# Kernel tuning notes

Measured on AMD Instinct MI355X. Metric: run time of the kernel, lower is better.

Reference implementation:

```python
import jax, jax.numpy as jnp
import numpy as np
import math

B, S_IN, S_OUT, D_IN, D_OUT, G = 8, 1024, 1024, 96, 96, 8
LN_EPS = 1e-5


def setup_inputs() -> dict:
    key = jax.random.key(0)
    k_x, k_m, k_p, k_l = jax.random.split(key, 4)
    x = jax.random.normal(k_x, (B, S_IN, D_IN), dtype=jnp.float32)
    M = jax.random.uniform(k_m, (D_OUT, D_IN), minval=-0.5, maxval=0.5, dtype=jnp.float32)
    P = jax.random.uniform(k_p, (D_OUT, D_OUT, G), minval=-0.1, maxval=0.1, dtype=jnp.float32)
    Linker = jax.random.uniform(k_l, (S_IN, S_OUT), minval=-0.1, maxval=0.1, dtype=jnp.float32)
    gamma = jnp.ones((D_OUT,), dtype=jnp.float32)
    beta = jnp.zeros((D_OUT,), dtype=jnp.float32)
    return {"x": x, "M": M, "P": P, "Linker": Linker, "gamma": gamma, "beta": beta}


def _layer_norm(z, gamma, beta):
    mu = jnp.mean(z, axis=-1, keepdims=True)
    var = jnp.mean(jnp.square(z - mu), axis=-1, keepdims=True)
    return (z - mu) * jax.lax.rsqrt(var + LN_EPS) * gamma + beta


def reference(x, M, P, Linker, gamma, beta):
    # Z = x @ M^T, then LayerNorm over feature dim
    Z0 = jnp.einsum('bsj,ij->bsi', x, M)           # (B, S_in, D_out)
    Z = _layer_norm(Z0, gamma, beta)
    # periods[i,j,g] = i*(D_out*G) + j*G + g + 2
    periods = (jnp.arange(D_OUT * D_OUT * G, dtype=jnp.float32)
               .reshape(D_OUT, D_OUT, G) + 2.0)
    k = jnp.arange(S_IN, dtype=jnp.float32)
    # phi[s,i,j,g] = cos(2*pi*s / periods[i,j,g])
    phi = jnp.cos((2.0 * math.pi) * k[:, None, None, None] / periods[None])
    # fuse basis reduction: W[s,i,j] = sum_g P[i,j,g] * phi[s,i,j,g]
    W = jnp.einsum('sijg,ijg->sij', phi, P)        # (S_in, D_out, D_out)
    # T[b,s,i] = sum_j Z[b,s,j] * W[s,i,j]
    T = jnp.einsum('bsj,sij->bsi', Z, W)           # (B, S_in, D_out)
    # sequence transform via Linker
    U = jnp.einsum('bsi,st->bti', T, Linker)       # (B, S_out, D_out)
    # shared residual: x @ M^T (pre-LN) through the same Linker
    residual = jnp.einsum('bsi,st->bti', Z0, Linker)
    return U + residual
```

## Files before the change

### kernel.cpp

```cpp
#include <hip/hip_runtime.h>
#include <cstdint>
#include <cstddef>

#define BSTRIDE 98304

typedef __attribute__((ext_vector_type(8))) short short8;
typedef __attribute__((ext_vector_type(4))) float f32x4;

__device__ __forceinline__ uint16_t f2bf(float x) {
    uint32_t u = __float_as_uint(x);
    return (uint16_t)((u + 0x7FFF + ((u >> 16) & 1)) >> 16);
}
__device__ __forceinline__ float bf2f(uint16_t b) {
    return __uint_as_float(((uint32_t)b) << 16);
}
__device__ __forceinline__ float cosrev(float x) {
    return __builtin_amdgcn_cosf(x);
}

union SmemA {
    struct {
        union {
            float M[96][97];
            struct { float zb[16][97]; float ps1[16][8];
                     float ps2[16][8]; float stats[16][2]; } ln;
        } m;
        float xs[16][96];
    } a;
    struct { float T[64][65]; } kl;
};

__global__ __launch_bounds__(384, 4) void kA(
    const float* __restrict__ x, const float* __restrict__ M,
    const float* __restrict__ L,
    const float* __restrict__ gamma, const float* __restrict__ beta,
    float* __restrict__ Z0, float* __restrict__ Z, uint16_t* __restrict__ Lt)
{
    __shared__ SmemA sm;
    const int t  = threadIdx.x;
    const int bx = blockIdx.x;

    if (bx >= 512) {
        const int bx2 = bx - 512;
        const int s0 = (bx2 & 15) * 64, t0 = (bx2 >> 4) * 64;
        if (t < 64) {
            for (int r = 0; r < 64; ++r)
                sm.kl.T[r][t] = L[(size_t)(s0 + r) * 1024 + t0 + t];
        }
        __syncthreads();
        if (t < 64) {
            uint16_t* orow = Lt + (size_t)(t0 + t) * 1024 + s0;
            #pragma unroll
            for (int c4 = 0; c4 < 16; ++c4) {
                uint32_t u01 = (uint32_t)f2bf(sm.kl.T[c4*4+0][t]) |
                               ((uint32_t)f2bf(sm.kl.T[c4*4+1][t]) << 16);
                uint32_t u23 = (uint32_t)f2bf(sm.kl.T[c4*4+2][t]) |
                               ((uint32_t)f2bf(sm.kl.T[c4*4+3][t]) << 16);
                uint2 o; o.x = u01; o.y = u23;
                *(uint2*)(orow + c4 * 4) = o;
            }
        }
        return;
    }

    const int R0 = bx * 16;
    const int b  = R0 >> 10;
    const int sb = R0 & 1023;

    #pragma unroll
    for (int k = 0; k < 6; ++k) {
        int mm = t + 384 * k;
        int i = mm / 24, j0 = (mm % 24) * 4;
        float4 v = *(const float4*)(M + (size_t)i * 96 + j0);
        sm.a.m.M[i][j0]   = v.x; sm.a.m.M[i][j0+1] = v.y;
        sm.a.m.M[i][j0+2] = v.z; sm.a.m.M[i][j0+3] = v.w;
    }
    {
        int row = t / 24, j0 = (t % 24) * 4;
        float4 v = *(const float4*)(x + (size_t)(R0 + row) * 96 + j0);
        *(float4*)&sm.a.xs[row][j0] = v;
    }
    __syncthreads();

    const int e = t % 96;
    const int q = t / 96;
    float acc[4] = {0.f, 0.f, 0.f, 0.f};
    for (int j0 = 0; j0 < 96; j0 += 4) {
        float m0 = sm.a.m.M[e][j0+0], m1 = sm.a.m.M[e][j0+1];
        float m2 = sm.a.m.M[e][j0+2], m3 = sm.a.m.M[e][j0+3];
        #pragma unroll
        for (int rr = 0; rr < 4; ++rr) {
            float4 xv = *(const float4*)&sm.a.xs[q * 4 + rr][j0];
            acc[rr] = fmaf(m0, xv.x, fmaf(m1, xv.y,
                      fmaf(m2, xv.z, fmaf(m3, xv.w, acc[rr]))));
        }
    }
    __syncthreads();
    #pragma unroll
    for (int rr = 0; rr < 4; ++rr) sm.a.m.ln.zb[q * 4 + rr][e] = acc[rr];
    __syncthreads();

    if (t < 128) {
        int r = t >> 3, seg = t & 7;
        float s1 = 0.f, s2 = 0.f;
        #pragma unroll
        for (int k = 0; k < 12; ++k) {
            float v = sm.a.m.ln.zb[r][seg * 12 + k];
            s1 += v; s2 += v * v;
        }
        sm.a.m.ln.ps1[r][seg] = s1; sm.a.m.ln.ps2[r][seg] = s2;
    }
    __syncthreads();
    if (t < 16) {
        float s1 = 0.f, s2 = 0.f;
        #pragma unroll
        for (int k = 0; k < 8; ++k) { s1 += sm.a.m.ln.ps1[t][k]; s2 += sm.a.m.ln.ps2[t][k]; }
        float mu  = s1 * (1.f / 96.f);
        float var = s2 * (1.f / 96.f) - mu * mu;
        sm.a.m.ln.stats[t][0] = mu;
        sm.a.m.ln.stats[t][1] = rsqrtf(var + 1e-5f);
    }
    __syncthreads();

    {
        float gm = gamma[e], bt = beta[e];
        #pragma unroll
        for (int rr = 0; rr < 4; ++rr) {
            int r = q * 4 + rr;
            float z  = acc[rr];
            float mu = sm.a.m.ln.stats[r][0], rs = sm.a.m.ln.stats[r][1];
            size_t o = (size_t)(sb + r) * 768 + (size_t)b * 96 + e;
            Z0[o] = z;
            Z[o]  = (z - mu) * rs * gm + bt;
        }
    }
}

struct SmemB {
    float    zs[8][8][100];
    uint16_t W[8][12][104];
    uint16_t stage[12][8][8];
};

__global__ __launch_bounds__(384, 4) void kB(
    const float* __restrict__ P, const float* __restrict__ Z,
    const float* __restrict__ Z0, uint16_t* __restrict__ Vt)
{
    __shared__ SmemB sm;
    const int t  = threadIdx.x;
    const int sg = blockIdx.x >> 3;
    const int ih = blockIdx.x & 7;
    const int s0 = sg * 8;
    const int i0 = ih * 12;

    #pragma unroll
    for (int k = 0; k < 4; ++k) {
        int c = t + 384 * k;
        int elem = c * 4;
        int sp = elem / 768, rem = elem - sp * 768;
        int bb = rem / 96,  j0 = rem - bb * 96;
        float4 v = *(const float4*)(Z + (size_t)s0 * 768 + elem);
        *(float4*)&sm.zs[sp][bb][j0] = v;
    }

    {
        const int j   = t % 96;
        const int iqb = t / 96;
        const float sf = (float)s0;
        #pragma unroll 1
        for (int kk = 0; kk < 3; ++kk) {
            const int ip = kk * 4 + iqb;
            const int ig = i0 + ip;
            const float* Pp = P + ((size_t)ig * 96 + j) * 8;
            float4 pa = *(const float4*)(Pp);
            float4 pb = *(const float4*)(Pp + 4);
            float pv[8] = {pa.x, pa.y, pa.z, pa.w, pb.x, pb.y, pb.z, pb.w};
            float base = (float)((ig * 96 + j) * 8 + 2);
            float c[8], cp[8], tc[8];
            #pragma unroll
            for (int g = 0; g < 8; ++g) {
                float inv = __builtin_amdgcn_rcpf(base + (float)g);
                tc[g] = 2.0f * cosrev(inv);
                c[g]  = cosrev(__builtin_amdgcn_fractf(sf * inv));
                cp[g] = cosrev(__builtin_amdgcn_fractf((sf - 1.0f) * inv));
            }
            #pragma unroll
            for (int sp = 0; sp < 8; ++sp) {
                float w = 0.f;
                #pragma unroll
                for (int g = 0; g < 8; ++g) w = fmaf(pv[g], c[g], w);
                sm.W[sp][ip][j] = f2bf(w);
                #pragma unroll
                for (int g = 0; g < 8; ++g) {
                    float cn = fmaf(tc[g], c[g], -cp[g]);
                    cp[g] = c[g]; c[g] = cn;
                }
            }
        }
    }
    __syncthreads();

    {
        const int s2  = t / 48;
        const int rem = t % 48;
        const int ipq = rem / 8;
        const int bb  = rem % 8;
        const int ia  = ipq * 2, ib = ia + 1;
        float accA = 0.f, accB = 0.f;
        const uint16_t* w0 = &sm.W[s2][ia][0];
        const uint16_t* w1 = &sm.W[s2][ib][0];
        const float*    zz = &sm.zs[s2][bb][0];
        #pragma unroll 3
        for (int j0 = 0; j0 < 96; j0 += 8) {
            short8 wa = *(const short8*)(w0 + j0);
            short8 wb = *(const short8*)(w1 + j0);
            float4 z0 = *(const float4*)(zz + j0);
            float4 z1 = *(const float4*)(zz + j0 + 4);
            accA = fmaf(bf2f((uint16_t)wa[0]), z0.x, accA);
            accB = fmaf(bf2f((uint16_t)wb[0]), z0.x, accB);
            accA = fmaf(bf2f((uint16_t)wa[1]), z0.y, accA);
            accB = fmaf(bf2f((uint16_t)wb[1]), z0.y, accB);
            accA = fmaf(bf2f((uint16_t)wa[2]), z0.z, accA);
            accB = fmaf(bf2f((uint16_t)wb[2]), z0.z, accB);
            accA = fmaf(bf2f((uint16_t)wa[3]), z0.w, accA);
            accB = fmaf(bf2f((uint16_t)wb[3]), z0.w, accB);
            accA = fmaf(bf2f((uint16_t)wa[4]), z1.x, accA);
            accB = fmaf(bf2f((uint16_t)wb[4]), z1.x, accB);
            accA = fmaf(bf2f((uint16_t)wa[5]), z1.y, accA);
            accB = fmaf(bf2f((uint16_t)wb[5]), z1.y, accB);
            accA = fmaf(bf2f((uint16_t)wa[6]), z1.z, accA);
            accB = fmaf(bf2f((uint16_t)wb[6]), z1.z, accB);
            accA = fmaf(bf2f((uint16_t)wa[7]), z1.w, accA);
            accB = fmaf(bf2f((uint16_t)wb[7]), z1.w, accB);
        }
        float2 r2 = *(const float2*)(Z0 + (size_t)(s0 + s2) * 768 + bb * 96 + i0 + ia);
        sm.stage[ia][bb][s2] = f2bf(accA + r2.x);
        sm.stage[ib][bb][s2] = f2bf(accB + r2.y);
    }
    __syncthreads();

    if (t < 96) {
        int ip = t >> 3, bb = t & 7;
        uint4 v = *(const uint4*)&sm.stage[ip][bb][0];
        *(uint4*)(Vt + ((size_t)bb * 96 + i0 + ip) * 1024 + s0) = v;
    }
}

__global__ __launch_bounds__(256, 4) void k3_mfma(
    const uint16_t* __restrict__ Lt, const uint16_t* __restrict__ Vt,
    float* __restrict__ out)
{
    __shared__ float racc[3][64][13];
    const int lane = threadIdx.x & 63;
    const int kw   = threadIdx.x >> 6;
    const int m    = lane & 15;
    const int quad = lane >> 4;
    const int t0   = blockIdx.x * 16;
    const int b    = blockIdx.y;
    const int ih   = blockIdx.z;

    const uint16_t* Lp = Lt + (size_t)(t0 + m) * 1024 + kw * 256 + quad * 8;
    const uint16_t* Vp = Vt + ((size_t)b * 96 + ih * 48 + m) * 1024 + kw * 256 + quad * 8;

    f32x4 acc[3];
    #pragma unroll
    for (int ii = 0; ii < 3; ++ii) acc[ii] = (f32x4){0.f, 0.f, 0.f, 0.f};

    short8 a = *(const short8*)Lp;
    short8 bv[3];
    #pragma unroll
    for (int ii = 0; ii < 3; ++ii)
        bv[ii] = *(const short8*)(Vp + (size_t)ii * 16 * 1024);

    for (int kc = 0; kc < 7; ++kc) {
        short8 an = *(const short8*)(Lp + (kc + 1) * 32);
        short8 bn[3];
        #pragma unroll
        for (int ii = 0; ii < 3; ++ii)
            bn[ii] = *(const short8*)(Vp + (size_t)ii * 16 * 1024 + (kc + 1) * 32);
        #pragma unroll
        for (int ii = 0; ii < 3; ++ii)
            acc[ii] = __builtin_amdgcn_mfma_f32_16x16x32_bf16(a, bv[ii], acc[ii], 0, 0, 0);
        a = an;
        #pragma unroll
        for (int ii = 0; ii < 3; ++ii) bv[ii] = bn[ii];
    }
    #pragma unroll
    for (int ii = 0; ii < 3; ++ii)
        acc[ii] = __builtin_amdgcn_mfma_f32_16x16x32_bf16(a, bv[ii], acc[ii], 0, 0, 0);

    if (kw > 0) {
        #pragma unroll
        for (int ii = 0; ii < 3; ++ii)
            #pragma unroll
            for (int r = 0; r < 4; ++r)
                racc[kw - 1][lane][ii * 4 + r] = acc[ii][r];
    }
    __syncthreads();
    if (kw == 0) {
        float* po = out + (size_t)b * BSTRIDE;
        #pragma unroll
        for (int ii = 0; ii < 3; ++ii)
            #pragma unroll
            for (int r = 0; r < 4; ++r)
                po[(size_t)(t0 + quad * 4 + r) * 96 + ih * 48 + ii * 16 + m] =
                    acc[ii][r] + racc[0][lane][ii * 4 + r] +
                    racc[1][lane][ii * 4 + r] + racc[2][lane][ii * 4 + r];
    }
}

extern "C" void kernel_launch(void* const* d_in, const int* in_sizes, int n_in,
                              void* d_out, int out_size, void* d_ws, size_t ws_size,
                              hipStream_t stream)
{
    const float* x     = (const float*)d_in[0];
    const float* M     = (const float*)d_in[1];
    const float* P     = (const float*)d_in[2];
    const float* Lnk   = (const float*)d_in[3];
    const float* gamma = (const float*)d_in[4];
    const float* beta  = (const float*)d_in[5];
    float* out = (float*)d_out;

    uint8_t* ws = (uint8_t*)d_ws;
    uint16_t* Lt = (uint16_t*)ws;
    uint16_t* Vt = (uint16_t*)(ws + 2097152);
    float*    Z0 = (float*)(ws + 3670016);
    float*    Z  = (float*)(ws + 6815744);

    kA<<<768, 384, 0, stream>>>(x, M, Lnk, gamma, beta, Z0, Z, Lt);
    kB<<<1024, 384, 0, stream>>>(P, Z, Z0, Vt);
    k3_mfma<<<dim3(64, 8, 2), 256, 0, stream>>>(Lt, Vt, out);
}
```

Baseline: 112.1 us.

## Fuse projection/LayerNorm kernel with W-basis contraction kernel via shared memory

Merges the x@M^T + LayerNorm kernel and the W-construction/contraction kernel into one kernel. Each block now handles 4 sequence positions across all 8 batches and half of the output features, so Z and Z0 stay in shared memory instead of going through global memory. This drops one launch and the Z/Z0 round trip. In exchange, M is reloaded and the projection recomputed per block pair, and the occupancy hint drops from 4 to 3 blocks per SM.

New measurement: 125.4 us. +11.9%, slower.

```diff
diff --git a/kernel.cpp b/kernel.cpp
--- a/kernel.cpp
+++ b/kernel.cpp
@@ -14,29 +14,27 @@
 __device__ __forceinline__ float bf2f(uint16_t b) {
     return __uint_as_float(((uint32_t)b) << 16);
 }
-__device__ __forceinline__ float cosrev(float x) {
-    return __builtin_amdgcn_cosf(x);
-}
-
-union SmemA {
+
+union SmemU {
     struct {
-        union {
-            float M[96][97];
-            struct { float zb[16][97]; float ps1[16][8];
-                     float ps2[16][8]; float stats[16][2]; } ln;
-        } m;
-        float xs[16][96];
-    } a;
+        union { float M[96][97]; uint16_t W[4][48][104]; } mw;
+        union { float xs[4][8][96]; uint16_t stage[48][8][4]; } xst;
+        float zr[4][8][97];
+        float zs[4][8][100];
+        float ps1[32][8];
+        float ps2[32][8];
+        float stats[32][2];
+    } c;
     struct { float T[64][65]; } kl;
 };
 
-__global__ __launch_bounds__(384, 4) void kA(
+__global__ __launch_bounds__(384, 3) void kAB(
     const float* __restrict__ x, const float* __restrict__ M,
-    const float* __restrict__ L,
+    const float* __restrict__ P, const float* __restrict__ L,
     const float* __restrict__ gamma, const float* __restrict__ beta,
-    float* __restrict__ Z0, float* __restrict__ Z, uint16_t* __restrict__ Lt)
+    uint16_t* __restrict__ Lt, uint16_t* __restrict__ Vt)
 {
-    __shared__ SmemA sm;
+    __shared__ SmemU sm;
     const int t  = threadIdx.x;
     const int bx = blockIdx.x;
 
@@ -63,133 +61,104 @@
         return;
     }
 
-    const int R0 = bx * 16;
-    const int b  = R0 >> 10;
-    const int sb = R0 & 1023;
+    const int gg = bx >> 1;
+    const int h  = bx & 1;
+    const int s0 = gg * 4;
+    const int i0 = h * 48;
 
     #pragma unroll
     for (int k = 0; k < 6; ++k) {
         int mm = t + 384 * k;
         int i = mm / 24, j0 = (mm % 24) * 4;
         float4 v = *(const float4*)(M + (size_t)i * 96 + j0);
-        sm.a.m.M[i][j0]   = v.x; sm.a.m.M[i][j0+1] = v.y;
-        sm.a.m.M[i][j0+2] = v.z; sm.a.m.M[i][j0+3] = v.w;
-    }
-    {
-        int row = t / 24, j0 = (t % 24) * 4;
-        float4 v = *(const float4*)(x + (size_t)(R0 + row) * 96 + j0);
-        *(float4*)&sm.a.xs[row][j0] = v;
+        sm.c.mw.M[i][j0]   = v.x; sm.c.mw.M[i][j0+1] = v.y;
+        sm.c.mw.M[i][j0+2] = v.z; sm.c.mw.M[i][j0+3] = v.w;
+    }
+    {
+        float4* xf = (float4*)&sm.c.xst.xs[0][0][0];
+        #pragma unroll
+        for (int r = 0; r < 2; ++r) {
+            int c = t + 384 * r;
+            int elem = c * 4;
+            int sp = elem / 768, rem = elem - sp * 768;
+            int bb = rem / 96,  j0 = rem - bb * 96;
+            xf[c] = *(const float4*)(x + (size_t)bb * BSTRIDE +
+                                     (size_t)(s0 + sp) * 96 + j0);
+        }
     }
     __syncthreads();
 
     const int e = t % 96;
     const int q = t / 96;
-    float acc[4] = {0.f, 0.f, 0.f, 0.f};
+    float acc[8] = {0.f,0.f,0.f,0.f,0.f,0.f,0.f,0.f};
     for (int j0 = 0; j0 < 96; j0 += 4) {
-        float m0 = sm.a.m.M[e][j0+0], m1 = sm.a.m.M[e][j0+1];
-        float m2 = sm.a.m.M[e][j0+2], m3 = sm.a.m.M[e][j0+3];
-        #pragma unroll
-        for (int rr = 0; rr < 4; ++rr) {
-            float4 xv = *(const float4*)&sm.a.xs[q * 4 + rr][j0];
-            acc[rr] = fmaf(m0, xv.x, fmaf(m1, xv.y,
-                      fmaf(m2, xv.z, fmaf(m3, xv.w, acc[rr]))));
-        }
-    }
-    __syncthreads();
-    #pragma unroll
-    for (int rr = 0; rr < 4; ++rr) sm.a.m.ln.zb[q * 4 + rr][e] = acc[rr];
-    __syncthreads();
-
-    if (t < 128) {
+        float m0 = sm.c.mw.M[e][j0+0], m1 = sm.c.mw.M[e][j0+1];
+        float m2 = sm.c.mw.M[e][j0+2], m3 = sm.c.mw.M[e][j0+3];
+        #pragma unroll
+        for (int bb = 0; bb < 8; ++bb) {
+            float4 xv = *(const float4*)&sm.c.xst.xs[q][bb][j0];
+            acc[bb] = fmaf(m0, xv.x, fmaf(m1, xv.y,
+                      fmaf(m2, xv.z, fmaf(m3, xv.w, acc[bb]))));
+        }
+    }
+    #pragma unroll
+    for (int bb = 0; bb < 8; ++bb) sm.c.zr[q][bb][e] = acc[bb];
+    __syncthreads();
+
+    if (t < 256) {
         int r = t >> 3, seg = t & 7;
+        const float* zp = &sm.c.zr[0][0][0] + r * 97 + seg * 12;
         float s1 = 0.f, s2 = 0.f;
         #pragma unroll
-        for (int k = 0; k < 12; ++k) {
-            float v = sm.a.m.ln.zb[r][seg * 12 + k];
-            s1 += v; s2 += v * v;
-        }
-        sm.a.m.ln.ps1[r][seg] = s1; sm.a.m.ln.ps2[r][seg] = s2;
-    }
-    __syncthreads();
-    if (t < 16) {
+        for (int k = 0; k < 12; ++k) { float v = zp[k]; s1 += v; s2 += v * v; }
+        sm.c.ps1[r][seg] = s1; sm.c.ps2[r][seg] = s2;
+    }
+    __syncthreads();
+    if (t < 32) {
         float s1 = 0.f, s2 = 0.f;
         #pragma unroll
-        for (int k = 0; k < 8; ++k) { s1 += sm.a.m.ln.ps1[t][k]; s2 += sm.a.m.ln.ps2[t][k]; }
+        for (int k = 0; k < 8; ++k) { s1 += sm.c.ps1[t][k]; s2 += sm.c.ps2[t][k]; }
         float mu  = s1 * (1.f / 96.f);
         float var = s2 * (1.f / 96.f) - mu * mu;
-        sm.a.m.ln.stats[t][0] = mu;
-        sm.a.m.ln.stats[t][1] = rsqrtf(var + 1e-5f);
+        sm.c.stats[t][0] = mu;
+        sm.c.stats[t][1] = rsqrtf(var + 1e-5f);
     }
     __syncthreads();
 
     {
         float gm = gamma[e], bt = beta[e];
         #pragma unroll
-        for (int rr = 0; rr < 4; ++rr) {
-            int r = q * 4 + rr;
-            float z  = acc[rr];
-            float mu = sm.a.m.ln.stats[r][0], rs = sm.a.m.ln.stats[r][1];
-            size_t o = (size_t)(sb + r) * 768 + (size_t)b * 96 + e;
-            Z0[o] = z;
-            Z[o]  = (z - mu) * rs * gm + bt;
-        }
-    }
-}
-
-struct SmemB {
-    float    zs[8][8][100];
-    uint16_t W[8][12][104];
-    uint16_t stage[12][8][8];
-};
-
-__global__ __launch_bounds__(384, 4) void kB(
-    const float* __restrict__ P, const float* __restrict__ Z,
-    const float* __restrict__ Z0, uint16_t* __restrict__ Vt)
-{
-    __shared__ SmemB sm;
-    const int t  = threadIdx.x;
-    const int sg = blockIdx.x >> 3;
-    const int ih = blockIdx.x & 7;
-    const int s0 = sg * 8;
-    const int i0 = ih * 12;
-
-    #pragma unroll
-    for (int k = 0; k < 4; ++k) {
-        int c = t + 384 * k;
-        int elem = c * 4;
-        int sp = elem / 768, rem = elem - sp * 768;
-        int bb = rem / 96,  j0 = rem - bb * 96;
-        float4 v = *(const float4*)(Z + (size_t)s0 * 768 + elem);
-        *(float4*)&sm.zs[sp][bb][j0] = v;
-    }
-
-    {
-        const int j   = t % 96;
-        const int iqb = t / 96;
-        const float sf = (float)s0;
-        #pragma unroll 1
-        for (int kk = 0; kk < 3; ++kk) {
-            const int ip = kk * 4 + iqb;
+        for (int bb = 0; bb < 8; ++bb) {
+            float mu = sm.c.stats[q * 8 + bb][0], rs = sm.c.stats[q * 8 + bb][1];
+            sm.c.zs[q][bb][e] = (acc[bb] - mu) * rs * gm + bt;
+        }
+    }
+    {
+        const float sf  = (float)s0;
+        const float sm1 = sf - 1.0f;
+        #pragma unroll 2
+        for (int kk = 0; kk < 12; ++kk) {
+            const int ip = kk * 4 + q;
             const int ig = i0 + ip;
-            const float* Pp = P + ((size_t)ig * 96 + j) * 8;
+            const float* Pp = P + ((size_t)ig * 96 + e) * 8;
             float4 pa = *(const float4*)(Pp);
             float4 pb = *(const float4*)(Pp + 4);
             float pv[8] = {pa.x, pa.y, pa.z, pa.w, pb.x, pb.y, pb.z, pb.w};
-            float base = (float)((ig * 96 + j) * 8 + 2);
+            float base = (float)((ig * 96 + e) * 8 + 2);
             float c[8], cp[8], tc[8];
             #pragma unroll
             for (int g = 0; g < 8; ++g) {
                 float inv = __builtin_amdgcn_rcpf(base + (float)g);
-                tc[g] = 2.0f * cosrev(inv);
-                c[g]  = cosrev(__builtin_amdgcn_fractf(sf * inv));
-                cp[g] = cosrev(__builtin_amdgcn_fractf((sf - 1.0f) * inv));
+                tc[g] = 2.0f * __builtin_amdgcn_cosf(inv);
+                c[g]  = __builtin_amdgcn_cosf(__builtin_amdgcn_fractf(sf  * inv));
+                cp[g] = __builtin_amdgcn_cosf(__builtin_amdgcn_fractf(sm1 * inv));
             }
             #pragma unroll
-            for (int sp = 0; sp < 8; ++sp) {
+            for (int sp = 0; sp < 4; ++sp) {
                 float w = 0.f;
                 #pragma unroll
                 for (int g = 0; g < 8; ++g) w = fmaf(pv[g], c[g], w);
-                sm.W[sp][ip][j] = f2bf(w);
+                sm.c.mw.W[sp][ip][e] = f2bf(w);
                 #pragma unroll
                 for (int g = 0; g < 8; ++g) {
                     float cn = fmaf(tc[g], c[g], -cp[g]);
@@ -201,48 +170,67 @@
     __syncthreads();
 
     {
-        const int s2  = t / 48;
-        const int rem = t % 48;
-        const int ipq = rem / 8;
-        const int bb  = rem % 8;
-        const int ia  = ipq * 2, ib = ia + 1;
-        float accA = 0.f, accB = 0.f;
-        const uint16_t* w0 = &sm.W[s2][ia][0];
-        const uint16_t* w1 = &sm.W[s2][ib][0];
-        const float*    zz = &sm.zs[s2][bb][0];
+        const int s2  = t / 96;
+        const int rem = t % 96;
+        const int ipq = rem >> 3;
+        const int bb  = rem & 7;
+        const int ia  = ipq * 4;
+        float a0 = 0.f, a1 = 0.f, a2 = 0.f, a3 = 0.f;
+        const uint16_t* w0 = &sm.c.mw.W[s2][ia][0];
+        const float*    zz = &sm.c.zs[s2][bb][0];
         #pragma unroll 3
         for (int j0 = 0; j0 < 96; j0 += 8) {
             short8 wa = *(const short8*)(w0 + j0);
-            short8 wb = *(const short8*)(w1 + j0);
+            short8 wb = *(const short8*)(w0 + 104 + j0);
+            short8 wc = *(const short8*)(w0 + 208 + j0);
+            short8 wd = *(const short8*)(w0 + 312 + j0);
             float4 z0 = *(const float4*)(zz + j0);
             float4 z1 = *(const float4*)(zz + j0 + 4);
-            accA = fmaf(bf2f((uint16_t)wa[0]), z0.x, accA);
-            accB = fmaf(bf2f((uint16_t)wb[0]), z0.x, accB);
-            accA = fmaf(bf2f((uint16_t)wa[1]), z0.y, accA);
-            accB = fmaf(bf2f((uint16_t)wb[1]), z0.y, accB);
-            accA = fmaf(bf2f((uint16_t)wa[2]), z0.z, accA);
-            accB = fmaf(bf2f((uint16_t)wb[2]), z0.z, accB);
-            accA = fmaf(bf2f((uint16_t)wa[3]), z0.w, accA);
-            accB = fmaf(bf2f((uint16_t)wb[3]), z0.w, accB);
-            accA = fmaf(bf2f((uint16_t)wa[4]), z1.x, accA);
-            accB = fmaf(bf2f((uint16_t)wb[4]), z1.x, accB);
-            accA = fmaf(bf2f((uint16_t)wa[5]), z1.y, accA);
-            accB = fmaf(bf2f((uint16_t)wb[5]), z1.y, accB);
-            accA = fmaf(bf2f((uint16_t)wa[6]), z1.z, accA);
-            accB = fmaf(bf2f((uint16_t)wb[6]), z1.z, accB);
-            accA = fmaf(bf2f((uint16_t)wa[7]), z1.w, accA);
-            accB = fmaf(bf2f((uint16_t)wb[7]), z1.w, accB);
-        }
-        float2 r2 = *(const float2*)(Z0 + (size_t)(s0 + s2) * 768 + bb * 96 + i0 + ia);
-        sm.stage[ia][bb][s2] = f2bf(accA + r2.x);
-        sm.stage[ib][bb][s2] = f2bf(accB + r2.y);
-    }
-    __syncthreads();
-
-    if (t < 96) {
+            a0 = fmaf(bf2f((uint16_t)wa[0]), z0.x, a0);
+            a1 = fmaf(bf2f((uint16_t)wb[0]), z0.x, a1);
+            a2 = fmaf(bf2f((uint16_t)wc[0]), z0.x, a2);
+            a3 = fmaf(bf2f((uint16_t)wd[0]), z0.x, a3);
+            a0 = fmaf(bf2f((uint16_t)wa[1]), z0.y, a0);
+            a1 = fmaf(bf2f((uint16_t)wb[1]), z0.y, a1);
+            a2 = fmaf(bf2f((uint16_t)wc[1]), z0.y, a2);
+            a3 = fmaf(bf2f((uint16_t)wd[1]), z0.y, a3);
+            a0 = fmaf(bf2f((uint16_t)wa[2]), z0.z, a0);
+            a1 = fmaf(bf2f((uint16_t)wb[2]), z0.z, a1);
+            a2 = fmaf(bf2f((uint16_t)wc[2]), z0.z, a2);
+            a3 = fmaf(bf2f((uint16_t)wd[2]), z0.z, a3);
+            a0 = fmaf(bf2f((uint16_t)wa[3]), z0.w, a0);
+            a1 = fmaf(bf2f((uint16_t)wb[3]), z0.w, a1);
+            a2 = fmaf(bf2f((uint16_t)wc[3]), z0.w, a2);
+            a3 = fmaf(bf2f((uint16_t)wd[3]), z0.w, a3);
+            a0 = fmaf(bf2f((uint16_t)wa[4]), z1.x, a0);
+            a1 = fmaf(bf2f((uint16_t)wb[4]), z1.x, a1);
+            a2 = fmaf(bf2f((uint16_t)wc[4]), z1.x, a2);
+            a3 = fmaf(bf2f((uint16_t)wd[4]), z1.x, a3);
+            a0 = fmaf(bf2f((uint16_t)wa[5]), z1.y, a0);
+            a1 = fmaf(bf2f((uint16_t)wb[5]), z1.y, a1);
+            a2 = fmaf(bf2f((uint16_t)wc[5]), z1.y, a2);
+            a3 = fmaf(bf2f((uint16_t)wd[5]), z1.y, a3);
+            a0 = fmaf(bf2f((uint16_t)wa[6]), z1.z, a0);
+            a1 = fmaf(bf2f((uint16_t)wb[6]), z1.z, a1);
+            a2 = fmaf(bf2f((uint16_t)wc[6]), z1.z, a2);
+            a3 = fmaf(bf2f((uint16_t)wd[6]), z1.z, a3);
+            a0 = fmaf(bf2f((uint16_t)wa[7]), z1.w, a0);
+            a1 = fmaf(bf2f((uint16_t)wb[7]), z1.w, a1);
+            a2 = fmaf(bf2f((uint16_t)wc[7]), z1.w, a2);
+            a3 = fmaf(bf2f((uint16_t)wd[7]), z1.w, a3);
+        }
+        const float* zrow = &sm.c.zr[s2][bb][i0 + ia];
+        sm.c.xst.stage[ia+0][bb][s2] = f2bf(a0 + zrow[0]);
+        sm.c.xst.stage[ia+1][bb][s2] = f2bf(a1 + zrow[1]);
+        sm.c.xst.stage[ia+2][bb][s2] = f2bf(a2 + zrow[2]);
+        sm.c.xst.stage[ia+3][bb][s2] = f2bf(a3 + zrow[3]);
+    }
+    __syncthreads();
+
+    {
         int ip = t >> 3, bb = t & 7;
-        uint4 v = *(const uint4*)&sm.stage[ip][bb][0];
-        *(uint4*)(Vt + ((size_t)bb * 96 + i0 + ip) * 1024 + s0) = v;
+        uint2 v = *(const uint2*)&sm.c.xst.stage[ip][bb][0];
+        *(uint2*)(Vt + ((size_t)bb * 96 + i0 + ip) * 1024 + s0) = v;
     }
 }
 
@@ -324,10 +312,7 @@
     uint8_t* ws = (uint8_t*)d_ws;
     uint16_t* Lt = (uint16_t*)ws;
     uint16_t* Vt = (uint16_t*)(ws + 2097152);
-    float*    Z0 = (float*)(ws + 3670016);
-    float*    Z  = (float*)(ws + 6815744);
-
-    kA<<<768, 384, 0, stream>>>(x, M, Lnk, gamma, beta, Z0, Z, Lt);
-    kB<<<1024, 384, 0, stream>>>(P, Z, Z0, Vt);
+
+    kAB    <<<768, 384, 0, stream>>>(x, M, P, Lnk, gamma, beta, Lt, Vt);
     k3_mfma<<<dim3(64, 8, 2), 256, 0, stream>>>(Lt, Vt, out);
 }
```

## Halve kB sequence tile, prefetch P/Z into registers, one output per thread

Applied to the files above, without the earlier changes.

kB now processes 4 sequence positions per block instead of 8, doubling the grid to 2048 blocks and raising the launch-bounds occupancy hint to 6. P coefficients and Z tiles are loaded into registers before the cosine recurrence so global latency overlaps the trig work. The residual load is issued before the barrier. The contraction now computes one output per thread with four independent accumulators, which breaks the FMA dependency chain. The trade-off is that the per-block cosine setup (rcp and cos per g) is amortized over fewer positions, so total trig work roughly doubles.

Result: slower. 135.9 us (+21.2%).

```diff
diff --git a/kernel.cpp b/kernel.cpp
--- a/kernel.cpp
+++ b/kernel.cpp
@@ -13,9 +13,6 @@
 }
 __device__ __forceinline__ float bf2f(uint16_t b) {
     return __uint_as_float(((uint32_t)b) << 16);
-}
-__device__ __forceinline__ float cosrev(float x) {
-    return __builtin_amdgcn_cosf(x);
 }
 
 union SmemA {
@@ -137,55 +134,60 @@
 }
 
 struct SmemB {
-    float    zs[8][8][100];
-    uint16_t W[8][12][104];
-    uint16_t stage[12][8][8];
+    float    zs[4][8][100];
+    uint16_t W[4][12][100];
+    uint16_t stage[12][8][4];
 };
 
-__global__ __launch_bounds__(384, 4) void kB(
+__global__ __launch_bounds__(384, 6) void kB(
     const float* __restrict__ P, const float* __restrict__ Z,
     const float* __restrict__ Z0, uint16_t* __restrict__ Vt)
 {
     __shared__ SmemB sm;
     const int t  = threadIdx.x;
-    const int sg = blockIdx.x >> 3;
-    const int ih = blockIdx.x & 7;
-    const int s0 = sg * 8;
+    const int sg = blockIdx.x & 255;
+    const int ih = blockIdx.x >> 8;
+    const int s0 = sg * 4;
     const int i0 = ih * 12;
 
-    #pragma unroll
-    for (int k = 0; k < 4; ++k) {
-        int c = t + 384 * k;
-        int elem = c * 4;
-        int sp = elem / 768, rem = elem - sp * 768;
-        int bb = rem / 96,  j0 = rem - bb * 96;
-        float4 v = *(const float4*)(Z + (size_t)s0 * 768 + elem);
-        *(float4*)&sm.zs[sp][bb][j0] = v;
+    const int j   = t % 96;
+    const int iqb = t / 96;
+
+    float4 pA[3], pB[3];
+    #pragma unroll
+    for (int kk = 0; kk < 3; ++kk) {
+        const int ig = i0 + kk * 4 + iqb;
+        const float* Pp = P + ((size_t)ig * 96 + j) * 8;
+        pA[kk] = *(const float4*)(Pp);
+        pB[kk] = *(const float4*)(Pp + 4);
+    }
+    float4 zreg[2];
+    #pragma unroll
+    for (int r = 0; r < 2; ++r) {
+        int c = t + 384 * r;
+        zreg[r] = *(const float4*)(Z + (size_t)s0 * 768 + (size_t)c * 4);
     }
 
     {
-        const int j   = t % 96;
-        const int iqb = t / 96;
-        const float sf = (float)s0;
+        const float sf  = (float)s0;
+        const float sm1 = sf - 1.0f;
         #pragma unroll 1
         for (int kk = 0; kk < 3; ++kk) {
             const int ip = kk * 4 + iqb;
             const int ig = i0 + ip;
-            const float* Pp = P + ((size_t)ig * 96 + j) * 8;
-            float4 pa = *(const float4*)(Pp);
-            float4 pb = *(const float4*)(Pp + 4);
-            float pv[8] = {pa.x, pa.y, pa.z, pa.w, pb.x, pb.y, pb.z, pb.w};
+            float pv[8] = {pA[kk].x, pA[kk].y, pA[kk].z, pA[kk].w,
+                           pB[kk].x, pB[kk].y, pB[kk].z, pB[kk].w};
             float base = (float)((ig * 96 + j) * 8 + 2);
             float c[8], cp[8], tc[8];
             #pragma unroll
             for (int g = 0; g < 8; ++g) {
                 float inv = __builtin_amdgcn_rcpf(base + (float)g);
-                tc[g] = 2.0f * cosrev(inv);
-                c[g]  = cosrev(__builtin_amdgcn_fractf(sf * inv));
-                cp[g] = cosrev(__builtin_amdgcn_fractf((sf - 1.0f) * inv));
+                tc[g] = 2.0f * __builtin_amdgcn_cosf(inv);
+                c[g]  = __builtin_amdgcn_cosf(__builtin_amdgcn_fractf(sf  * inv));
+                cp[g] = __builtin_amdgcn_cosf(__builtin_amdgcn_fractf(sm1 * inv));
             }
             #pragma unroll
-            for (int sp = 0; sp < 8; ++sp) {
+            for (int sp = 0; sp < 4; ++sp) {
                 float w = 0.f;
                 #pragma unroll
                 for (int g = 0; g < 8; ++g) w = fmaf(pv[g], c[g], w);
@@ -198,51 +200,51 @@
             }
         }
     }
+
+    #pragma unroll
+    for (int r = 0; r < 2; ++r) {
+        int c = t + 384 * r;
+        int elem = c * 4;
+        int sp = elem / 768;
+        int rem = elem - sp * 768;
+        int bb = rem / 96, j0 = rem - bb * 96;
+        *(float4*)&sm.zs[sp][bb][j0] = zreg[r];
+    }
+
+    const int s2   = t / 96;
+    const int rem2 = t % 96;
+    const int ipq  = rem2 >> 3;
+    const int bb2  = rem2 & 7;
+    float res = Z0[(size_t)(s0 + s2) * 768 + (size_t)bb2 * 96 + i0 + ipq];
     __syncthreads();
 
     {
-        const int s2  = t / 48;
-        const int rem = t % 48;
-        const int ipq = rem / 8;
-        const int bb  = rem % 8;
-        const int ia  = ipq * 2, ib = ia + 1;
-        float accA = 0.f, accB = 0.f;
-        const uint16_t* w0 = &sm.W[s2][ia][0];
-        const uint16_t* w1 = &sm.W[s2][ib][0];
-        const float*    zz = &sm.zs[s2][bb][0];
+        float a0 = 0.f, a1 = 0.f, a2 = 0.f, a3 = 0.f;
+        const uint16_t* w0 = &sm.W[s2][ipq][0];
+        const float*    zz = &sm.zs[s2][bb2][0];
         #pragma unroll 3
         for (int j0 = 0; j0 < 96; j0 += 8) {
             short8 wa = *(const short8*)(w0 + j0);
-            short8 wb = *(const short8*)(w1 + j0);
-            float4 z0 = *(const float4*)(zz + j0);
-            float4 z1 = *(const float4*)(zz + j0 + 4);
-            accA = fmaf(bf2f((uint16_t)wa[0]), z0.x, accA);
-            accB = fmaf(bf2f((uint16_t)wb[0]), z0.x, accB);
-            accA = fmaf(bf2f((uint16_t)wa[1]), z0.y, accA);
-            accB = fmaf(bf2f((uint16_t)wb[1]), z0.y, accB);
-            accA = fmaf(bf2f((uint16_t)wa[2]), z0.z, accA);
-            accB = fmaf(bf2f((uint16_t)wb[2]), z0.z, accB);
-            accA = fmaf(bf2f((uint16_t)wa[3]), z0.w, accA);
-            accB = fmaf(bf2f((uint16_t)wb[3]), z0.w, accB);
-            accA = fmaf(bf2f((uint16_t)wa[4]), z1.x, accA);
-            accB = fmaf(bf2f((uint16_t)wb[4]), z1.x, accB);
-            accA = fmaf(bf2f((uint16_t)wa[5]), z1.y, accA);
-            accB = fmaf(bf2f((uint16_t)wb[5]), z1.y, accB);
-            accA = fmaf(bf2f((uint16_t)wa[6]), z1.z, accA);
-            accB = fmaf(bf2f((uint16_t)wb[6]), z1.z, accB);
-            accA = fmaf(bf2f((uint16_t)wa[7]), z1.w, accA);
-            accB = fmaf(bf2f((uint16_t)wb[7]), z1.w, accB);
-        }
-        float2 r2 = *(const float2*)(Z0 + (size_t)(s0 + s2) * 768 + bb * 96 + i0 + ia);
-        sm.stage[ia][bb][s2] = f2bf(accA + r2.x);
-        sm.stage[ib][bb][s2] = f2bf(accB + r2.y);
+            float4 z0v = *(const float4*)(zz + j0);
+            float4 z1v = *(const float4*)(zz + j0 + 4);
+            a0 = fmaf(bf2f((uint16_t)wa[0]), z0v.x, a0);
+            a1 = fmaf(bf2f((uint16_t)wa[1]), z0v.y, a1);
+            a2 = fmaf(bf2f((uint16_t)wa[2]), z0v.z, a2);
+            a3 = fmaf(bf2f((uint16_t)wa[3]), z0v.w, a3);
+            a0 = fmaf(bf2f((uint16_t)wa[4]), z1v.x, a0);
+            a1 = fmaf(bf2f((uint16_t)wa[5]), z1v.y, a1);
+            a2 = fmaf(bf2f((uint16_t)wa[6]), z1v.z, a2);
+            a3 = fmaf(bf2f((uint16_t)wa[7]), z1v.w, a3);
+        }
+        float acc = (a0 + a1) + (a2 + a3);
+        sm.stage[ipq][bb2][s2] = f2bf(acc + res);
     }
     __syncthreads();
 
     if (t < 96) {
         int ip = t >> 3, bb = t & 7;
-        uint4 v = *(const uint4*)&sm.stage[ip][bb][0];
-        *(uint4*)(Vt + ((size_t)bb * 96 + i0 + ip) * 1024 + s0) = v;
+        uint2 v = *(const uint2*)&sm.stage[ip][bb][0];
+        *(uint2*)(Vt + ((size_t)bb * 96 + i0 + ip) * 1024 + s0) = v;
     }
 }
 
@@ -328,6 +330,6 @@
     float*    Z  = (float*)(ws + 6815744);
 
     kA<<<768, 384, 0, stream>>>(x, M, Lnk, gamma, beta, Z0, Z, Lt);
-    kB<<<1024, 384, 0, stream>>>(P, Z, Z0, Vt);
+    kB<<<2048, 384, 0, stream>>>(P, Z, Z0, Vt);
     k3_mfma<<<dim3(64, 8, 2), 256, 0, stream>>>(Lt, Vt, out);
 }
```
